# Performance work log

Hardware: AMD Instinct MI355X
Metric: run time of the kernel (lower is better)

## Reference

```python
import jax, jax.numpy as jnp
import numpy as np

M = 8192          # tokens
DIM = 2048        # per-stream width; K = 4*DIM
S = 4             # fixed stream count (Stream4 kernels)
N = 32            # fixed GEMM output width
SINKHORN_ITERS = 20


def setup_inputs() -> dict:
    key = jax.random.key(0)
    k1, k2 = jax.random.split(key)
    X = jax.random.normal(k1, (M, S * DIM), dtype=jnp.float32)
    # scale W so H = X @ W is O(1): keeps sigmoid/exp/sinkhorn numerically sane
    W = jax.random.normal(k2, (S * DIM, N), dtype=jnp.float32) / np.float32(np.sqrt(S * DIM))
    # module init: beta = zeros(24), alpha = ones(3), concatenated
    alpha_beta = jnp.concatenate([jnp.zeros(24, jnp.float32), jnp.ones(3, jnp.float32)])
    return {"X": X, "W": W, "alpha_beta": alpha_beta}


def _sinkhorn(P, iters=SINKHORN_ITERS):
    # doubly-stochastic normalization of [M, S, S] matrices
    for _ in range(iters):
        P = P / jnp.sum(P, axis=-1, keepdims=True)  # row normalize
        P = P / jnp.sum(P, axis=-2, keepdims=True)  # col normalize
    return P


def reference(X, W, alpha_beta):
    Mm, K = X.shape
    d = K // S
    # skinny GEMM producing the mixing logits (fused w/ SplitK in the kernel)
    H = X @ W                                   # [M, 32]
    b_res, b_pre, b_pos = alpha_beta[0:16], alpha_beta[16:20], alpha_beta[20:24]
    a_res, a_pre, a_pos = alpha_beta[24], alpha_beta[25], alpha_beta[26]
    H_pre = a_pre * jax.nn.sigmoid(H[:, 16:20]) + b_pre          # [M, 4]
    H_pos = a_pos * jax.nn.sigmoid(H[:, 20:24]) + b_pos          # [M, 4]
    H_res = (a_res * H[:, 0:16] + b_res).reshape(Mm, S, S)       # [M, 4, 4]
    H_res = _sinkhorn(jnp.exp(H_res))                            # doubly stochastic
    # view X as 4 streams of width d
    Xs = X.reshape(Mm, S, d)                                     # [M, 4, d]
    # ApplyPreTransform: collapse streams with H_pre weights
    Y = jnp.einsum('ms,msd->md', H_pre, Xs)                      # [M, d]
    # ApplyResidual: per-token 4x4 stream mix + broadcast of pre-transformed feature
    O = jnp.einsum('msi,mid->msd', H_res, Xs) + H_pos[:, :, None] * Y[:, None, :]
    return O.reshape(Mm, K)
```

## Files before the change

### kernel.cpp

```cpp
#include <hip/hip_runtime.h>
#include <math.h>
#include <stdint.h>

#define K_DIM 8192
#define D_DIM 2048
#define M_ROWS 8192
#define N_W 32
#define NC 24
#define KSPLIT 8
#define KRANGE (K_DIM / KSPLIT)
#define NKSTEP (KRANGE / 32)
#define TOTAL_KSTEPS (K_DIM / 32)

typedef short bf16x8 __attribute__((ext_vector_type(8)));
typedef float f32x4 __attribute__((ext_vector_type(4)));
union U32x4 { uint32_t u[4]; bf16x8 v; };

#define WFRAG_IDX(ks, tile, hilo) ((((ks) * 2 + (tile)) * 2 + (hilo)) * 64)

__global__ __launch_bounds__(256) void mhc_prepack_kernel(
    const float* __restrict__ W, unsigned short* __restrict__ wfrag,
    float* __restrict__ Hsum)
{
    const int idx = blockIdx.x * 256 + threadIdx.x;
    const int k = idx >> 5, n = idx & 31;
    const float w = W[(size_t)k * N_W + n];
    const uint32_t u = __float_as_uint(w);
    const float hif = __uint_as_float(u & 0xFFFF0000u);
    const uint32_t ur = __float_as_uint(w - hif);

    const int ks = k >> 5, kk = k & 31;
    const int lane = ((kk >> 3) << 4) | (n & 15);
    const int e = kk & 7;
    const int tile = n >> 4;
    unsigned short* p = wfrag + ((size_t)WFRAG_IDX(ks, tile, 0) + lane) * 8 + e;
    p[0]   = (unsigned short)(u >> 16);
    p[512] = (unsigned short)(ur >> 16);

    if (idx < M_ROWS * NC) Hsum[idx] = 0.f;
}

__global__ __launch_bounds__(256) void mhc_gemm_kernel(
    const float* __restrict__ X, const unsigned short* __restrict__ wfrag,
    float* __restrict__ Hsum)
{
    const int t = threadIdx.x;
    const int l = t & 63;
    const int wv = t >> 6;
    const int rowbase = blockIdx.x * 64;
    const int ks0 = blockIdx.y * NKSTEP;

    f32x4 c0 = {0.f, 0.f, 0.f, 0.f};
    f32x4 c1 = {0.f, 0.f, 0.f, 0.f};

    const int arow = rowbase + wv * 16 + (l & 15);
    const float* __restrict__ xrow = X + (size_t)arow * K_DIM + ((l >> 4) * 8);
    const bf16x8* __restrict__ wf = reinterpret_cast<const bf16x8*>(wfrag);

#pragma unroll 2
    for (int s = 0; s < NKSTEP; ++s) {
        const int ks = ks0 + s;
        const float* xc = xrow + ks * 32;
        const float4 xa = *reinterpret_cast<const float4*>(xc);
        const float4 xb = *reinterpret_cast<const float4*>(xc + 4);
        float xs[8];
        xs[0] = xa.x; xs[1] = xa.y; xs[2] = xa.z; xs[3] = xa.w;
        xs[4] = xb.x; xs[5] = xb.y; xs[6] = xb.z; xs[7] = xb.w;

        U32x4 ah, al;
#pragma unroll
        for (int p = 0; p < 4; ++p) {
            const uint32_t u0 = __float_as_uint(xs[2 * p]);
            const uint32_t u1 = __float_as_uint(xs[2 * p + 1]);
            const float h0 = __uint_as_float(u0 & 0xFFFF0000u);
            const float h1 = __uint_as_float(u1 & 0xFFFF0000u);
            const uint32_t r0 = __float_as_uint(xs[2 * p] - h0);
            const uint32_t r1 = __float_as_uint(xs[2 * p + 1] - h1);
            ah.u[p] = (u1 & 0xFFFF0000u) | (u0 >> 16);
            al.u[p] = (r1 & 0xFFFF0000u) | (r0 >> 16);
        }

        const bf16x8 bh0 = wf[WFRAG_IDX(ks, 0, 0) + l];
        const bf16x8 bl0 = wf[WFRAG_IDX(ks, 0, 1) + l];
        const bf16x8 bh1 = wf[WFRAG_IDX(ks, 1, 0) + l];
        const bf16x8 bl1 = wf[WFRAG_IDX(ks, 1, 1) + l];

        c0 = __builtin_amdgcn_mfma_f32_16x16x32_bf16(ah.v, bh0, c0, 0, 0, 0);
        c0 = __builtin_amdgcn_mfma_f32_16x16x32_bf16(al.v, bh0, c0, 0, 0, 0);
        c0 = __builtin_amdgcn_mfma_f32_16x16x32_bf16(ah.v, bl0, c0, 0, 0, 0);
        c1 = __builtin_amdgcn_mfma_f32_16x16x32_bf16(ah.v, bh1, c1, 0, 0, 0);
        c1 = __builtin_amdgcn_mfma_f32_16x16x32_bf16(al.v, bh1, c1, 0, 0, 0);
        c1 = __builtin_amdgcn_mfma_f32_16x16x32_bf16(ah.v, bl1, c1, 0, 0, 0);
    }

    const int drow = rowbase + wv * 16 + (l >> 4) * 4;
    const int col = l & 15;
#pragma unroll
    for (int r = 0; r < 4; ++r)
        atomicAdd(&Hsum[(size_t)(drow + r) * NC + col], c0[r]);
    if (col < 8) {
#pragma unroll
        for (int r = 0; r < 4; ++r)
            atomicAdd(&Hsum[(size_t)(drow + r) * NC + 16 + col], c1[r]);
    }
}

__global__ __launch_bounds__(256) void mhc_apply_kernel(
    const float* __restrict__ X, const float* __restrict__ Hsum,
    const float* __restrict__ ab, float* __restrict__ out)
{
    __shared__ float pbuf[NC];
    const int row = blockIdx.x;
    const int t = threadIdx.x;

    if (t < 64) {
        const int lane = t;
        const float pl = (lane < NC) ? Hsum[(size_t)row * NC + lane] : 0.f;
        const float bias  = (lane < NC) ? ab[lane] : 0.f;
        const float scale = ab[(lane < 16) ? 24 : ((lane < 20) ? 25 : 26)];

        float vout;
        if (lane < 16) {
            vout = __expf(fmaf(scale, pl, bias));
        } else {
            vout = fmaf(scale, 1.f / (1.f + __expf(-pl)), bias);
        }

        float p = vout;
        for (int it = 0; it < 20; ++it) {
            float rs = p + __shfl_xor(p, 1);
            rs += __shfl_xor(rs, 2);
            p = p / rs;
            float cs = p + __shfl_xor(p, 4);
            cs += __shfl_xor(cs, 8);
            p = p / cs;
        }
        if (lane < NC) pbuf[lane] = (lane < 16) ? p : vout;
    }
    __syncthreads();

    float hres[4][4], hpre[4], hpos[4];
#pragma unroll
    for (int i = 0; i < 16; ++i) hres[i >> 2][i & 3] = pbuf[i];
#pragma unroll
    for (int i = 0; i < 4; ++i) hpre[i] = pbuf[16 + i];
#pragma unroll
    for (int i = 0; i < 4; ++i) hpos[i] = pbuf[20 + i];

    const float4* __restrict__ Xr =
        reinterpret_cast<const float4*>(X + (size_t)row * K_DIM);
    float4* __restrict__ Or = reinterpret_cast<float4*>(out + (size_t)row * K_DIM);

#pragma unroll
    for (int q = 0; q < 2; ++q) {
        const int pos = t + q * 256;
        float4 xq[4];
#pragma unroll
        for (int i = 0; i < 4; ++i) xq[i] = Xr[i * (D_DIM / 4) + pos];

        float y[4];
#pragma unroll
        for (int e = 0; e < 4; ++e) {
            float s = 0.f;
#pragma unroll
            for (int i = 0; i < 4; ++i)
                s = fmaf(hpre[i], reinterpret_cast<const float*>(&xq[i])[e], s);
            y[e] = s;
        }

#pragma unroll
        for (int s = 0; s < 4; ++s) {
            float4 o;
            float* oe = reinterpret_cast<float*>(&o);
#pragma unroll
            for (int e = 0; e < 4; ++e) {
                float v = hpos[s] * y[e];
#pragma unroll
                for (int i = 0; i < 4; ++i)
                    v = fmaf(hres[s][i], reinterpret_cast<const float*>(&xq[i])[e], v);
                oe[e] = v;
            }
            Or[s * (D_DIM / 4) + pos] = o;
        }
    }
}

extern "C" void kernel_launch(void* const* d_in, const int* in_sizes, int n_in,
                              void* d_out, int out_size, void* d_ws, size_t ws_size,
                              hipStream_t stream) {
    const float* X  = (const float*)d_in[0];
    const float* W  = (const float*)d_in[1];
    const float* ab = (const float*)d_in[2];
    float* out = (float*)d_out;
    float* Hsum = (float*)d_ws;
    unsigned short* wfrag = (unsigned short*)((char*)d_ws + (size_t)M_ROWS * NC * 4);

    mhc_prepack_kernel<<<(K_DIM * N_W) / 256, 256, 0, stream>>>(W, wfrag, Hsum);
    dim3 g1(M_ROWS / 64, KSPLIT);
    mhc_gemm_kernel<<<g1, 256, 0, stream>>>(X, wfrag, Hsum);
    mhc_apply_kernel<<<M_ROWS, 256, 0, stream>>>(X, Hsum, ab, out);
}
```

Before: 183.4 us.

## Restructure split-K GEMM with LDS-staged prefetch and single-bf16 weights

The skinny GEMM now gives each block 16 rows and splits the block's K range across its four waves. Each wave prefetches the next X tile and weight fragments into registers, then stages X through an XOR-swizzled, double-buffered per-wave LDS buffer. Weights are round-to-nearest bf16 with no low residual, so each k-step issues 4 MFMAs instead of 6. The aim is better latency hiding and fewer MFMAs. In exchange, H loses some precision, and there are four times as many atomicAdds into the H accumulator.

```diff
diff --git a/kernel.cpp b/kernel.cpp
--- a/kernel.cpp
+++ b/kernel.cpp
@@ -8,15 +8,15 @@
 #define N_W 32
 #define NC 24
 #define KSPLIT 8
-#define KRANGE (K_DIM / KSPLIT)
-#define NKSTEP (KRANGE / 32)
-#define TOTAL_KSTEPS (K_DIM / 32)
+#define ROWS 16
+#define THR 256
+#define ITERS 8
 
 typedef short bf16x8 __attribute__((ext_vector_type(8)));
 typedef float f32x4 __attribute__((ext_vector_type(4)));
 union U32x4 { uint32_t u[4]; bf16x8 v; };
 
-#define WFRAG_IDX(ks, tile, hilo) ((((ks) * 2 + (tile)) * 2 + (hilo)) * 64)
+#define WFI(ks, tile) (((ks) * 2 + (tile)) * 64)
 
 __global__ __launch_bounds__(256) void mhc_prepack_kernel(
     const float* __restrict__ W, unsigned short* __restrict__ wfrag,
@@ -26,43 +26,61 @@
     const int k = idx >> 5, n = idx & 31;
     const float w = W[(size_t)k * N_W + n];
     const uint32_t u = __float_as_uint(w);
-    const float hif = __uint_as_float(u & 0xFFFF0000u);
-    const uint32_t ur = __float_as_uint(w - hif);
+    const uint32_t r = u + 0x7FFFu + ((u >> 16) & 1u);
 
     const int ks = k >> 5, kk = k & 31;
     const int lane = ((kk >> 3) << 4) | (n & 15);
     const int e = kk & 7;
     const int tile = n >> 4;
-    unsigned short* p = wfrag + ((size_t)WFRAG_IDX(ks, tile, 0) + lane) * 8 + e;
-    p[0]   = (unsigned short)(u >> 16);
-    p[512] = (unsigned short)(ur >> 16);
+    wfrag[((size_t)WFI(ks, tile) + lane) * 8 + e] = (unsigned short)(r >> 16);
 
     if (idx < M_ROWS * NC) Hsum[idx] = 0.f;
 }
 
-__global__ __launch_bounds__(256) void mhc_gemm_kernel(
+__global__ __launch_bounds__(THR) void mhc_gemm_kernel(
     const float* __restrict__ X, const unsigned short* __restrict__ wfrag,
     float* __restrict__ Hsum)
 {
+    __shared__ __align__(16) float4 Xl[4][2][128];
     const int t = threadIdx.x;
     const int l = t & 63;
     const int wv = t >> 6;
-    const int rowbase = blockIdx.x * 64;
-    const int ks0 = blockIdx.y * NKSTEP;
+    const int rowbase = blockIdx.x * ROWS;
+    const int ks0 = blockIdx.y * 32 + wv * ITERS;
+
+    const float4* __restrict__ Xg = reinterpret_cast<const float4*>(X);
+    const bf16x8* __restrict__ wf = reinterpret_cast<const bf16x8*>(wfrag);
+
+    const int lr = l >> 3;
+    const int lu = l & 7;
+    const int arow = l & 15;
+    const int au = (l >> 4) * 2;
 
     f32x4 c0 = {0.f, 0.f, 0.f, 0.f};
     f32x4 c1 = {0.f, 0.f, 0.f, 0.f};
-
-    const int arow = rowbase + wv * 16 + (l & 15);
-    const float* __restrict__ xrow = X + (size_t)arow * K_DIM + ((l >> 4) * 8);
-    const bf16x8* __restrict__ wf = reinterpret_cast<const bf16x8*>(wfrag);
-
-#pragma unroll 2
-    for (int s = 0; s < NKSTEP; ++s) {
-        const int ks = ks0 + s;
-        const float* xc = xrow + ks * 32;
-        const float4 xa = *reinterpret_cast<const float4*>(xc);
-        const float4 xb = *reinterpret_cast<const float4*>(xc + 4);
+    float4 pa, pb;
+    bf16x8 b0n, b1n;
+
+    pa = Xg[(size_t)(rowbase + lr) * (K_DIM / 4) + ks0 * 8 + lu];
+    pb = Xg[(size_t)(rowbase + 8 + lr) * (K_DIM / 4) + ks0 * 8 + lu];
+    b0n = wf[WFI(ks0, 0) + l];
+    b1n = wf[WFI(ks0, 1) + l];
+    Xl[wv][0][lr * 8 + (lu ^ lr)] = pa;
+    Xl[wv][0][(8 + lr) * 8 + (lu ^ lr)] = pb;
+
+#pragma unroll
+    for (int i = 0; i < ITERS; ++i) {
+        const bf16x8 b0 = b0n, b1 = b1n;
+        if (i + 1 < ITERS) {
+            const int ks = ks0 + i + 1;
+            pa = Xg[(size_t)(rowbase + lr) * (K_DIM / 4) + ks * 8 + lu];
+            pb = Xg[(size_t)(rowbase + 8 + lr) * (K_DIM / 4) + ks * 8 + lu];
+            b0n = wf[WFI(ks, 0) + l];
+            b1n = wf[WFI(ks, 1) + l];
+        }
+
+        const float4 xa = Xl[wv][i & 1][arow * 8 + (au ^ (arow & 7))];
+        const float4 xb = Xl[wv][i & 1][arow * 8 + ((au + 1) ^ (arow & 7))];
         float xs[8];
         xs[0] = xa.x; xs[1] = xa.y; xs[2] = xa.z; xs[3] = xa.w;
         xs[4] = xb.x; xs[5] = xb.y; xs[6] = xb.z; xs[7] = xb.w;
@@ -80,20 +98,18 @@
             al.u[p] = (r1 & 0xFFFF0000u) | (r0 >> 16);
         }
 
-        const bf16x8 bh0 = wf[WFRAG_IDX(ks, 0, 0) + l];
-        const bf16x8 bl0 = wf[WFRAG_IDX(ks, 0, 1) + l];
-        const bf16x8 bh1 = wf[WFRAG_IDX(ks, 1, 0) + l];
-        const bf16x8 bl1 = wf[WFRAG_IDX(ks, 1, 1) + l];
-
-        c0 = __builtin_amdgcn_mfma_f32_16x16x32_bf16(ah.v, bh0, c0, 0, 0, 0);
-        c0 = __builtin_amdgcn_mfma_f32_16x16x32_bf16(al.v, bh0, c0, 0, 0, 0);
-        c0 = __builtin_amdgcn_mfma_f32_16x16x32_bf16(ah.v, bl0, c0, 0, 0, 0);
-        c1 = __builtin_amdgcn_mfma_f32_16x16x32_bf16(ah.v, bh1, c1, 0, 0, 0);
-        c1 = __builtin_amdgcn_mfma_f32_16x16x32_bf16(al.v, bh1, c1, 0, 0, 0);
-        c1 = __builtin_amdgcn_mfma_f32_16x16x32_bf16(ah.v, bl1, c1, 0, 0, 0);
-    }
-
-    const int drow = rowbase + wv * 16 + (l >> 4) * 4;
+        c0 = __builtin_amdgcn_mfma_f32_16x16x32_bf16(ah.v, b0, c0, 0, 0, 0);
+        c0 = __builtin_amdgcn_mfma_f32_16x16x32_bf16(al.v, b0, c0, 0, 0, 0);
+        c1 = __builtin_amdgcn_mfma_f32_16x16x32_bf16(ah.v, b1, c1, 0, 0, 0);
+        c1 = __builtin_amdgcn_mfma_f32_16x16x32_bf16(al.v, b1, c1, 0, 0, 0);
+
+        if (i + 1 < ITERS) {
+            Xl[wv][(i + 1) & 1][lr * 8 + (lu ^ lr)] = pa;
+            Xl[wv][(i + 1) & 1][(8 + lr) * 8 + (lu ^ lr)] = pb;
+        }
+    }
+
+    const int drow = rowbase + ((l >> 4) << 2);
     const int col = l & 15;
 #pragma unroll
     for (int r = 0; r < 4; ++r)
@@ -192,11 +208,11 @@
     const float* W  = (const float*)d_in[1];
     const float* ab = (const float*)d_in[2];
     float* out = (float*)d_out;
-    float* Hsum = (float*)d_ws;
-    unsigned short* wfrag = (unsigned short*)((char*)d_ws + (size_t)M_ROWS * NC * 4);
+    unsigned short* wfrag = (unsigned short*)d_ws;
+    float* Hsum = (float*)((char*)d_ws + 524288);
 
     mhc_prepack_kernel<<<(K_DIM * N_W) / 256, 256, 0, stream>>>(W, wfrag, Hsum);
-    dim3 g1(M_ROWS / 64, KSPLIT);
-    mhc_gemm_kernel<<<g1, 256, 0, stream>>>(X, wfrag, Hsum);
+    dim3 g1(M_ROWS / ROWS, KSPLIT);
+    mhc_gemm_kernel<<<g1, THR, 0, stream>>>(X, wfrag, Hsum);
     mhc_apply_kernel<<<M_ROWS, 256, 0, stream>>>(X, Hsum, ab, out);
 }
```

After: 173.1 us. -5.6%, faster.
